# Kernel tuning notes

Measured on AMD Instinct MI355X. Metric: run time of the kernel, lower is better.

## Reference

```python
import jax, jax.numpy as jnp
import numpy as np

B, SQ, SK, D, H = 4, 2048, 2048, 1024, 16
EPS = 1e-6  # flax LayerNorm default


def layer_norm(x, g, b):
    m = x.mean(-1, keepdims=True)
    var = ((x - m) ** 2).mean(-1, keepdims=True)
    return (x - m) * jax.lax.rsqrt(var + EPS) * g + b


def setup_inputs() -> dict:
    key = jax.random.key(0)
    ks = jax.random.split(key, 16)
    s = 1.0 / np.sqrt(D).astype(np.float32)
    inp = {
        'q': jax.random.normal(ks[0], (B, SQ, D), jnp.float32),
        'k': jax.random.normal(ks[1], (B, SK, D), jnp.float32),
        'v': jax.random.normal(ks[2], (B, SK, D), jnp.float32),
        'mask': jax.random.randint(ks[3], (B, SK), 0, 2).astype(bool),
        'Wq': jax.random.normal(ks[4], (D, D), jnp.float32) * s,
        'bq': jnp.zeros((D,), jnp.float32),
        'Wk': jax.random.normal(ks[5], (D, D), jnp.float32) * s,
        'bk': jnp.zeros((D,), jnp.float32),
        'Wv': jax.random.normal(ks[6], (D, D), jnp.float32) * s,
        'bv': jnp.zeros((D,), jnp.float32),
        'Wo': jax.random.normal(ks[7], (D, D), jnp.float32) * s,
        'bo': jnp.zeros((D,), jnp.float32),
        'g1': jnp.ones((D,), jnp.float32),
        'b1': jnp.zeros((D,), jnp.float32),
        'g2': jnp.ones((D,), jnp.float32),
        'b2': jnp.zeros((D,), jnp.float32),
    }
    return inp


def reference(q, k, v, mask, Wq, bq, Wk, bk, Wv, bv, Wo, bo, g1, b1, g2, b2):
    qp = q @ Wq + bq                      # [B, SQ, D]
    kp = k @ Wk + bk                      # [B, SK, D]
    vp = v @ Wv + bv
    qh = qp.reshape(B, SQ, H, D // H)     # head = slice of last dim (matches scatter)
    kh = kp.reshape(B, SK, H, D // H)
    vh = vp.reshape(B, SK, H, D // H)
    # NOTE: original scales by sqrt(dim_out) (full dim), not head dim
    logits = jnp.einsum('bqhd,bkhd->bhqk', qh, kh) / np.sqrt(D).astype(np.float32)
    m = mask[:, None, None, :]            # [B,1,1,SK] broadcast over heads & queries
    A = jax.nn.softmax(jnp.where(m, logits, -jnp.inf), axis=-1)
    A = jnp.where(jnp.isnan(A), 0.0, A)   # fully-masked rows -> 0 (as in original)
    attn = jnp.einsum('bhqk,bkhd->bqhd', A, vh).reshape(B, SQ, D)  # gather heads
    x = layer_norm(qp + attn, g1, b1)
    out = layer_norm(x + jax.nn.relu(x @ Wo + bo), g2, b2)
    return out
```

## Files before the change

### kernel.cpp

```cpp
#include <hip/hip_runtime.h>

#define B_   4
#define SQS  2048
#define SKS  2048
#define DM   1024
#define H_   16
#define MT   8192

typedef __attribute__((ext_vector_type(8))) short bf16x8;
typedef __attribute__((ext_vector_type(4))) float f32x4;

__device__ __forceinline__ float bf2f(unsigned int u) { return __uint_as_float(u << 16); }
__device__ __forceinline__ unsigned short f2bf(float f) {
  unsigned int u = __float_as_uint(f);
  return (unsigned short)((u + 0x7fffu + ((u >> 16) & 1u)) >> 16);
}
__device__ __forceinline__ unsigned int pk_bf16(float a, float b) {
  return __builtin_amdgcn_perm(__float_as_uint(b) + 0x8000u,
                               __float_as_uint(a) + 0x8000u, 0x07060302u);
}
__device__ __forceinline__ unsigned int pk_trunc(float a, float b) {
  return __builtin_amdgcn_perm(__float_as_uint(b), __float_as_uint(a), 0x07060302u);
}
__device__ __forceinline__ float fexp2(float x) {
#if __has_builtin(__builtin_amdgcn_exp2f)
  return __builtin_amdgcn_exp2f(x);
#else
  return __expf(x * 0.69314718056f);
#endif
}
__device__ __forceinline__ void async16(const void* g, void* l) {
  __builtin_amdgcn_global_load_lds((const __attribute__((address_space(1))) unsigned int*)g,
                                   (__attribute__((address_space(3))) unsigned int*)l,
                                   16, 0, 0);
}

#define KSCALE 0.0450842200f
#define BIAS_UNMASKED 0.0028151213f

__global__ __launch_bounds__(256)
void prep_all(const float* __restrict__ q, const float* __restrict__ k,
              const float* __restrict__ v, const int* __restrict__ mask,
              const float* __restrict__ Wq, const float* __restrict__ Wk,
              const float* __restrict__ Wv, const float* __restrict__ Wo,
              unsigned short* __restrict__ qi, unsigned short* __restrict__ ki,
              unsigned short* __restrict__ vi,
              unsigned short* __restrict__ Wqt, unsigned short* __restrict__ Wkt,
              unsigned short* __restrict__ Wvt, unsigned short* __restrict__ Wot,
              float* __restrict__ mskb)
{
  __shared__ float s[32][33];
  const int bx = blockIdx.x, tid = threadIdx.x;
  if (bx < 24576) {
    const int which = bx >> 13, i = bx & 8191;
    const float* src = (which == 0) ? q : (which == 1) ? k : v;
    unsigned short* dst = (which == 0) ? qi : (which == 1) ? ki : vi;
    size_t o = ((size_t)i * 256 + tid) * 4;
    float4 f = *(const float4*)(src + o);
    uint2 u;
    u.x = pk_bf16(f.x, f.y);
    u.y = pk_bf16(f.z, f.w);
    *(uint2*)(dst + o) = u;
  } else if (bx < 28672) {
    const int idx = bx - 24576;
    const int w = idx >> 10, t = idx & 1023;
    const int n0 = (t & 31) * 32, k0 = (t >> 5) * 32;
    const float* W = (w == 0) ? Wq : (w == 1) ? Wk : (w == 2) ? Wv : Wo;
    unsigned short* Wt = (w == 0) ? Wqt : (w == 1) ? Wkt : (w == 2) ? Wvt : Wot;
#pragma unroll
    for (int p = 0; p < 4; p++) {
      int c = p * 256 + tid;
      int r = c >> 5, cc = c & 31;
      s[r][cc] = W[(size_t)(k0 + r) * DM + n0 + cc];
    }
    __syncthreads();
#pragma unroll
    for (int p = 0; p < 4; p++) {
      int c = p * 256 + tid;
      int r = c >> 5, cc = c & 31;
      Wt[(size_t)(n0 + r) * DM + k0 + cc] = f2bf(s[cc][r]);
    }
  } else {
    int i = (bx - 28672) * 256 + tid;
    mskb[i] = mask[i] ? BIAS_UNMASKED : -1e30f;
  }
}

__global__ __launch_bounds__(256)
void qkv_gemm(const unsigned short* __restrict__ A0, const unsigned short* __restrict__ A1,
              const unsigned short* __restrict__ A2,
              const unsigned short* __restrict__ W0, const unsigned short* __restrict__ W1,
              const unsigned short* __restrict__ W2,
              const float* __restrict__ s0, const float* __restrict__ s1,
              const float* __restrict__ s2,
              unsigned short* __restrict__ o0, unsigned short* __restrict__ o1,
              unsigned short* __restrict__ vT)
{
  const int L = blockIdx.x + (blockIdx.y << 3) + (blockIdx.z << 9);
  const int g = L & 7, i5 = L >> 3;
  const int nblk = i5 & 7;
  const int yz = (i5 >> 3) + g * 24;
  const int mblk = yz & 63;
  const int z = yz >> 6;

  const unsigned short* A  = (z == 0) ? A0 : (z == 1) ? A1 : A2;
  const unsigned short* Wt = (z == 0) ? W0 : (z == 1) ? W1 : W2;
  const float* bias        = (z == 0) ? s0 : (z == 1) ? s1 : s2;

  __shared__ short As[128 * 64];
  __shared__ short Bs[128 * 64];
  const int tid = threadIdx.x;
  const int m0 = mblk * 128, n0 = nblk * 128;
  const int wave = tid >> 6, ln = tid & 15, qd = (tid & 63) >> 4;
  const int wm = (wave >> 1) * 64, wn = (wave & 1) * 64;

  int srow[4], sgj[4];
#pragma unroll
  for (int u = 0; u < 4; u++) {
    int c = u * 256 + tid;
    srow[u] = c >> 3;
    sgj[u] = ((c & 7) ^ (srow[u] & 7)) * 8;
  }

  f32x4 acc[4][4];
  const f32x4 vzero = {0.f, 0.f, 0.f, 0.f};
#pragma unroll
  for (int i = 0; i < 4; i++)
#pragma unroll
    for (int j = 0; j < 4; j++) acc[i][j] = vzero;

  for (int k0 = 0; k0 < DM; k0 += 64) {
    __syncthreads();
#pragma unroll
    for (int u = 0; u < 4; u++) {
      int c = u * 256 + tid;
      async16(A  + (size_t)(m0 + srow[u]) * DM + k0 + sgj[u], (char*)As + c * 16);
      async16(Wt + (size_t)(n0 + srow[u]) * DM + k0 + sgj[u], (char*)Bs + c * 16);
    }
    __syncthreads();

#pragma unroll
    for (int kk = 0; kk < 2; kk++) {
      const int ch = ((kk * 4 + qd) ^ (ln & 7)) * 8;
      bf16x8 af[4], bfr[4];
#pragma unroll
      for (int i = 0; i < 4; i++)
        af[i] = *(const bf16x8*)(As + (wm + i * 16 + ln) * 64 + ch);
#pragma unroll
      for (int j = 0; j < 4; j++)
        bfr[j] = *(const bf16x8*)(Bs + (wn + j * 16 + ln) * 64 + ch);
#pragma unroll
      for (int i = 0; i < 4; i++)
#pragma unroll
        for (int j = 0; j < 4; j++)
          acc[i][j] = __builtin_amdgcn_mfma_f32_16x16x32_bf16(af[i], bfr[j], acc[i][j], 0, 0, 0);
    }
  }

  if (z != 2) {
    unsigned short* C = (z == 0) ? o0 : o1;
    const float sc = (z == 1) ? KSCALE : 1.0f;
#pragma unroll
    for (int j = 0; j < 4; j++) {
      int col = n0 + wn + j * 16 + ln;
      float bj = bias[col];
#pragma unroll
      for (int i = 0; i < 4; i++) {
        int row = m0 + wm + i * 16 + qd * 4;
#pragma unroll
        for (int r = 0; r < 4; r++)
          C[(size_t)(row + r) * DM + col] = f2bf((acc[i][j][r] + bj) * sc);
      }
    }
  } else {
#pragma unroll
    for (int j = 0; j < 4; j++) {
      int col = n0 + wn + j * 16 + ln;
      int h = col >> 6, d = col & 63;
      float bj = bias[col];
#pragma unroll
      for (int i = 0; i < 4; i++) {
        int tok0 = m0 + wm + i * 16 + qd * 4;
        int bb = tok0 >> 11;
        int kcol = ((tok0 & 2047) & ~63) + (i & 1) * 32 + qd * 8 + ((i >> 1) & 1) * 4;
        uint2 u;
        u.x = pk_bf16(acc[i][j][0] + bj, acc[i][j][1] + bj);
        u.y = pk_bf16(acc[i][j][2] + bj, acc[i][j][3] + bj);
        *(uint2*)(vT + ((size_t)(bb * H_ + h) * 64 + d) * SKS + kcol) = u;
      }
    }
  }
}

__global__ __launch_bounds__(256)
void gemm_bf16(const unsigned short* __restrict__ A,
               const unsigned short* __restrict__ Wt,
               const float* __restrict__ bias,
               unsigned short* __restrict__ C,
               int relu)
{
  const int L = blockIdx.x + (blockIdx.y << 3);
  const int g = L & 7, i5 = L >> 3;
  const int nblk = i5 & 7;
  const int mblk = (i5 >> 3) + (g << 3);

  __shared__ short As[128 * 64];
  __shared__ short Bs[128 * 64];
  const int tid = threadIdx.x;
  const int m0 = mblk * 128, n0 = nblk * 128;
  const int wave = tid >> 6, ln = tid & 15, qd = (tid & 63) >> 4;
  const int wm = (wave >> 1) * 64, wn = (wave & 1) * 64;

  int srow[4], sgj[4];
#pragma unroll
  for (int u = 0; u < 4; u++) {
    int c = u * 256 + tid;
    srow[u] = c >> 3;
    sgj[u] = ((c & 7) ^ (srow[u] & 7)) * 8;
  }

  f32x4 acc[4][4];
  const f32x4 vzero = {0.f, 0.f, 0.f, 0.f};
#pragma unroll
  for (int i = 0; i < 4; i++)
#pragma unroll
    for (int j = 0; j < 4; j++) acc[i][j] = vzero;

  for (int k0 = 0; k0 < DM; k0 += 64) {
    __syncthreads();
#pragma unroll
    for (int u = 0; u < 4; u++) {
      int c = u * 256 + tid;
      async16(A  + (size_t)(m0 + srow[u]) * DM + k0 + sgj[u], (char*)As + c * 16);
      async16(Wt + (size_t)(n0 + srow[u]) * DM + k0 + sgj[u], (char*)Bs + c * 16);
    }
    __syncthreads();

#pragma unroll
    for (int kk = 0; kk < 2; kk++) {
      const int ch = ((kk * 4 + qd) ^ (ln & 7)) * 8;
      bf16x8 af[4], bfr[4];
#pragma unroll
      for (int i = 0; i < 4; i++)
        af[i] = *(const bf16x8*)(As + (wm + i * 16 + ln) * 64 + ch);
#pragma unroll
      for (int j = 0; j < 4; j++)
        bfr[j] = *(const bf16x8*)(Bs + (wn + j * 16 + ln) * 64 + ch);
#pragma unroll
      for (int i = 0; i < 4; i++)
#pragma unroll
        for (int j = 0; j < 4; j++)
          acc[i][j] = __builtin_amdgcn_mfma_f32_16x16x32_bf16(af[i], bfr[j], acc[i][j], 0, 0, 0);
    }
  }

#pragma unroll
  for (int j = 0; j < 4; j++) {
    int col = n0 + wn + j * 16 + ln;
    float bj = bias[col];
#pragma unroll
    for (int i = 0; i < 4; i++) {
      int row = m0 + wm + i * 16 + qd * 4;
#pragma unroll
      for (int r = 0; r < 4; r++) {
        float v = acc[i][j][r] + bj;
        if (relu) v = fmaxf(v, 0.f);
        C[(size_t)(row + r) * DM + col] = f2bf(v);
      }
    }
  }
}

__global__ __launch_bounds__(256, 2)
void attn_fwd(const unsigned short* __restrict__ qp,
              const unsigned short* __restrict__ kp,
              const unsigned short* __restrict__ vT,
              const float* __restrict__ maskb,
              unsigned short* __restrict__ attn)
{
  __shared__ short Ks[128 * 64];
  __shared__ short Vs[64 * 128];
  __shared__ float bias_s[128];

  const int tid = threadIdx.x;
  const int L = blockIdx.x + (blockIdx.y << 3) + (blockIdx.z << 7);
  const int g = L & 7, i5 = L >> 3;
  const int qblk = i5 & 7;
  const int bh = (i5 >> 3) + (g << 3);
  const int h = bh & 15, b = bh >> 4;
  const int q0 = qblk * 256;
  const int wave = tid >> 6, ln = tid & 15, qd = (tid & 63) >> 4;

  int kRow[4], kOff[4], vRow[4], vOff[4];
#pragma unroll
  for (int u = 0; u < 4; u++) {
    int c = u * 256 + tid;
    kRow[u] = c >> 3;
    kOff[u] = ((c & 7) ^ (kRow[u] & 7)) * 8;
    vRow[u] = c >> 4;
    int j = c & 15;
    vOff[u] = ((j & 8) | ((j ^ vRow[u]) & 7)) * 8;
  }

  const unsigned short* kbase = kp + (size_t)(b * SKS) * DM + (h << 6);
  const unsigned short* vbase = vT + (size_t)((b * H_ + h) * 64) * SKS;

  bf16x8 qf[4][2];
#pragma unroll
  for (int gq = 0; gq < 4; gq++) {
    const unsigned short* qrow =
        qp + (size_t)(b * SQS + q0 + wave * 64 + gq * 16 + ln) * DM + (h << 6);
    qf[gq][0] = *(const bf16x8*)(qrow + qd * 8);
    qf[gq][1] = *(const bf16x8*)(qrow + 32 + qd * 8);
  }

  union { bf16x8 v; unsigned int u[4]; } onesf;
  onesf.u[0] = onesf.u[1] = onesf.u[2] = onesf.u[3] = 0x3F803F80u;

  const f32x4 vzero = {0.f, 0.f, 0.f, 0.f};
  f32x4 oA[4][4], lacc[4];
#pragma unroll
  for (int gq = 0; gq < 4; gq++) {
    lacc[gq] = vzero;
#pragma unroll
    for (int t = 0; t < 4; t++) oA[gq][t] = vzero;
  }

  for (int kt = 0; kt < SKS / 128; kt++) {
    const int k0 = kt * 128;
    __syncthreads();
    if (tid < 128) bias_s[tid] = maskb[b * SKS + k0 + tid];
#pragma unroll
    for (int u = 0; u < 4; u++) {
      int c = u * 256 + tid;
      async16(kbase + (size_t)(k0 + kRow[u]) * DM + kOff[u], (char*)Ks + c * 16);
      async16(vbase + (size_t)vRow[u] * SKS + k0 + vOff[u], (char*)Vs + c * 16);
    }
    __syncthreads();

#pragma unroll
    for (int h2 = 0; h2 < 2; h2++) {
      bf16x8 kf[4][2];
      f32x4 btv[4];
#pragma unroll
      for (int t = 0; t < 4; t++) {
        const short* krow = Ks + (h2 * 64 + t * 16 + ln) * 64;
        kf[t][0] = *(const bf16x8*)(krow + ((0 + qd) ^ (ln & 7)) * 8);
        kf[t][1] = *(const bf16x8*)(krow + ((4 + qd) ^ (ln & 7)) * 8);
        btv[t] = *(const f32x4*)(bias_s + h2 * 64 + t * 16 + qd * 4);
      }

      bf16x8 pf[4][2];
#pragma unroll
      for (int gq = 0; gq < 4; gq++) {
        f32x4 sS[4];
#pragma unroll
        for (int t = 0; t < 4; t++) {
          f32x4 a = __builtin_amdgcn_mfma_f32_16x16x32_bf16(kf[t][0], qf[gq][0], btv[t], 0, 0, 0);
          sS[t]   = __builtin_amdgcn_mfma_f32_16x16x32_bf16(kf[t][1], qf[gq][1], a,      0, 0, 0);
        }
        float p[4][4];
#pragma unroll
        for (int t = 0; t < 4; t++) {
          p[t][0] = fexp2(sS[t][0]);
          p[t][1] = fexp2(sS[t][1]);
          p[t][2] = fexp2(sS[t][2]);
          p[t][3] = fexp2(sS[t][3]);
        }
        union { bf16x8 v; unsigned int u[4]; } P0, P1;
        P0.u[0] = pk_trunc(p[0][0], p[0][1]);
        P0.u[1] = pk_trunc(p[0][2], p[0][3]);
        P0.u[2] = pk_trunc(p[2][0], p[2][1]);
        P0.u[3] = pk_trunc(p[2][2], p[2][3]);
        P1.u[0] = pk_trunc(p[1][0], p[1][1]);
        P1.u[1] = pk_trunc(p[1][2], p[1][3]);
        P1.u[2] = pk_trunc(p[3][0], p[3][1]);
        P1.u[3] = pk_trunc(p[3][2], p[3][3]);
        pf[gq][0] = P0.v;
        pf[gq][1] = P1.v;
        lacc[gq] = __builtin_amdgcn_mfma_f32_16x16x32_bf16(pf[gq][0], onesf.v, lacc[gq], 0, 0, 0);
        lacc[gq] = __builtin_amdgcn_mfma_f32_16x16x32_bf16(pf[gq][1], onesf.v, lacc[gq], 0, 0, 0);
      }

#pragma unroll
      for (int t2 = 0; t2 < 4; t2++) {
        const short* vrow = Vs + (t2 * 16 + ln) * 128;
        bf16x8 vf0 = *(const bf16x8*)(vrow + (h2 * 8 + ((0 + qd) ^ (ln & 7))) * 8);
        bf16x8 vf1 = *(const bf16x8*)(vrow + (h2 * 8 + ((4 + qd) ^ (ln & 7))) * 8);
#pragma unroll
        for (int gq = 0; gq < 4; gq++) {
          oA[gq][t2] = __builtin_amdgcn_mfma_f32_16x16x32_bf16(pf[gq][0], vf0, oA[gq][t2], 0, 0, 0);
          oA[gq][t2] = __builtin_amdgcn_mfma_f32_16x16x32_bf16(pf[gq][1], vf1, oA[gq][t2], 0, 0, 0);
        }
      }
    }
  }

#pragma unroll
  for (int gq = 0; gq < 4; gq++) {
    float linv[4];
#pragma unroll
    for (int r = 0; r < 4; r++)
      linv[r] = (lacc[gq][r] > 0.f) ? 1.0f / lacc[gq][r] : 0.f;
#pragma unroll
    for (int t2 = 0; t2 < 4; t2++)
#pragma unroll
      for (int r = 0; r < 4; r++) {
        size_t idx = (size_t)(b * SQS + q0 + wave * 64 + gq * 16 + qd * 4 + r) * DM
                   + (h << 6) + t2 * 16 + ln;
        attn[idx] = f2bf(oA[gq][t2][r] * linv[r]);
      }
  }
}

__global__ __launch_bounds__(256)
void ln_fuse(const unsigned short* __restrict__ Xa, const unsigned short* __restrict__ Xb,
             const float* __restrict__ gamma, const float* __restrict__ beta,
             unsigned short* __restrict__ outb, float* __restrict__ outf, int mode)
{
  const int row = blockIdx.x, tid = threadIdx.x;
  const size_t base = (size_t)row * DM + tid * 4;
  uint2 ua = *(const uint2*)(Xa + base);
  uint2 ub = *(const uint2*)(Xb + base);
  float v0 = bf2f(ua.x & 0xffffu) + bf2f(ub.x & 0xffffu);
  float v1 = bf2f(ua.x >> 16)     + bf2f(ub.x >> 16);
  float v2 = bf2f(ua.y & 0xffffu) + bf2f(ub.y & 0xffffu);
  float v3 = bf2f(ua.y >> 16)     + bf2f(ub.y >> 16);
  float s  = (v0 + v1) + (v2 + v3);
  float s2 = (v0 * v0 + v1 * v1) + (v2 * v2 + v3 * v3);
#pragma unroll
  for (int off = 1; off < 64; off <<= 1) {
    s  += __shfl_xor(s, off);
    s2 += __shfl_xor(s2, off);
  }
  __shared__ float red[8];
  if ((tid & 63) == 0) { red[tid >> 6] = s; red[4 + (tid >> 6)] = s2; }
  __syncthreads();
  float S  = (red[0] + red[1]) + (red[2] + red[3]);
  float S2 = (red[4] + red[5]) + (red[6] + red[7]);
  float mean = S * (1.0f / 1024.0f);
  float var  = S2 * (1.0f / 1024.0f) - mean * mean;
  float rstd = rsqrtf(var + 1e-6f);
  int c = tid * 4;
  float o0 = (v0 - mean) * rstd * gamma[c + 0] + beta[c + 0];
  float o1 = (v1 - mean) * rstd * gamma[c + 1] + beta[c + 1];
  float o2 = (v2 - mean) * rstd * gamma[c + 2] + beta[c + 2];
  float o3 = (v3 - mean) * rstd * gamma[c + 3] + beta[c + 3];
  if (mode == 0) {
    uint2 o;
    o.x = (unsigned)f2bf(o0) | ((unsigned)f2bf(o1) << 16);
    o.y = (unsigned)f2bf(o2) | ((unsigned)f2bf(o3) << 16);
    *(uint2*)(outb + base) = o;
  } else {
    float4 o = {o0, o1, o2, o3};
    *(float4*)(outf + base) = o;
  }
}

extern "C" void kernel_launch(void* const* d_in, const int* in_sizes, int n_in,
                              void* d_out, int out_size, void* d_ws, size_t ws_size,
                              hipStream_t stream)
{
  (void)in_sizes; (void)n_in; (void)out_size; (void)ws_size;
  const float* q    = (const float*)d_in[0];
  const float* k    = (const float*)d_in[1];
  const float* v    = (const float*)d_in[2];
  const int*   mask = (const int*)  d_in[3];
  const float* Wq   = (const float*)d_in[4];
  const float* bq   = (const float*)d_in[5];
  const float* Wk   = (const float*)d_in[6];
  const float* bk   = (const float*)d_in[7];
  const float* Wv   = (const float*)d_in[8];
  const float* bv   = (const float*)d_in[9];
  const float* Wo   = (const float*)d_in[10];
  const float* bo   = (const float*)d_in[11];
  const float* g1   = (const float*)d_in[12];
  const float* b1   = (const float*)d_in[13];
  const float* g2   = (const float*)d_in[14];
  const float* b2   = (const float*)d_in[15];

  char* ws = (char*)d_ws;
  const size_t SZ16 = (size_t)16 << 20;
  unsigned short* qi   = (unsigned short*)(ws + 0 * SZ16);
  unsigned short* ki   = (unsigned short*)(ws + 1 * SZ16);
  unsigned short* vi   = (unsigned short*)(ws + 2 * SZ16);
  unsigned short* qpb  = (unsigned short*)(ws + 3 * SZ16);
  unsigned short* kpb  = (unsigned short*)(ws + 4 * SZ16);
  unsigned short* vTb  = (unsigned short*)(ws + 6 * SZ16);
  unsigned short* Wqt  = (unsigned short*)(ws + 7 * SZ16 + ((size_t)0 << 20));
  unsigned short* Wkt  = (unsigned short*)(ws + 7 * SZ16 + ((size_t)2 << 20));
  unsigned short* Wvt  = (unsigned short*)(ws + 7 * SZ16 + ((size_t)4 << 20));
  unsigned short* Wot  = (unsigned short*)(ws + 7 * SZ16 + ((size_t)6 << 20));
  float*          mskb = (float*)         (ws + 7 * SZ16 + ((size_t)8 << 20));
  unsigned short* attnb = qi;
  unsigned short* xb    = ki;
  unsigned short* hb    = vi;

  prep_all     <<<28704,            256, 0, stream>>>(q, k, v, mask, Wq, Wk, Wv, Wo,
                                                      qi, ki, vi, Wqt, Wkt, Wvt, Wot, mskb);

  qkv_gemm     <<<dim3(8, 64, 3),   256, 0, stream>>>(qi, ki, vi, Wqt, Wkt, Wvt,
                                                      bq, bk, bv, qpb, kpb, vTb);

  attn_fwd     <<<dim3(8, 16, 4),   256, 0, stream>>>(qpb, kpb, vTb, mskb, attnb);

  ln_fuse      <<<8192,             256, 0, stream>>>(qpb, attnb, g1, b1, xb, nullptr, 0);
  gemm_bf16    <<<dim3(8, 64),      256, 0, stream>>>(xb, Wot, bo, hb, 1);
  ln_fuse      <<<8192,             256, 0, stream>>>(xb, hb, g2, b2, nullptr, (float*)d_out, 1);
}
```

Before: 347.4 us.

## Split attention over two key halves and merge partials in layernorm

The attention kernel now splits the key sequence into two halves, launching twice as many blocks. Each block writes an unnormalized bf16 partial output and its row sums to workspace. The first layernorm kernel becomes a merge kernel that adds both partials, divides by the combined sum and applies layernorm. This is meant to raise parallelism and occupancy in attention (launch bounds raised to 4 blocks per CU), at the cost of extra partial-output traffic. Since no running max is used, the partials combine exactly, but rounding the unnormalized partials to bf16 may lose some precision.

After: 759.1 us. 119% more time.

```diff
diff --git a/kernel.cpp b/kernel.cpp
--- a/kernel.cpp
+++ b/kernel.cpp
@@ -271,24 +271,28 @@
   }
 }
 
-__global__ __launch_bounds__(256, 2)
+__global__ __launch_bounds__(256, 4)
 void attn_fwd(const unsigned short* __restrict__ qp,
               const unsigned short* __restrict__ kp,
               const unsigned short* __restrict__ vT,
               const float* __restrict__ maskb,
-              unsigned short* __restrict__ attn)
+              unsigned short* __restrict__ O0,
+              unsigned short* __restrict__ O1,
+              float* __restrict__ lws)
 {
   __shared__ short Ks[128 * 64];
   __shared__ short Vs[64 * 128];
   __shared__ float bias_s[128];
 
   const int tid = threadIdx.x;
-  const int L = blockIdx.x + (blockIdx.y << 3) + (blockIdx.z << 7);
+  const int L = blockIdx.x + (blockIdx.y << 4) + (blockIdx.z << 8);
   const int g = L & 7, i5 = L >> 3;
-  const int qblk = i5 & 7;
-  const int bh = (i5 >> 3) + (g << 3);
+  const int half = i5 & 1;
+  const int qblk = (i5 >> 1) & 7;
+  const int bh = (i5 >> 4) + (g << 3);
   const int h = bh & 15, b = bh >> 4;
   const int q0 = qblk * 256;
+  const int koff0 = half * (SKS / 2);
   const int wave = tid >> 6, ln = tid & 15, qd = (tid & 63) >> 4;
 
   int kRow[4], kOff[4], vRow[4], vOff[4];
@@ -326,8 +330,8 @@
     for (int t = 0; t < 4; t++) oA[gq][t] = vzero;
   }
 
-  for (int kt = 0; kt < SKS / 128; kt++) {
-    const int k0 = kt * 128;
+  for (int kt = 0; kt < SKS / 2 / 128; kt++) {
+    const int k0 = koff0 + kt * 128;
     __syncthreads();
     if (tid < 128) bias_s[tid] = maskb[b * SKS + k0 + tid];
 #pragma unroll
@@ -396,36 +400,49 @@
     }
   }
 
+  unsigned short* obuf = half ? O1 : O0;
+  float* lbuf = lws + (size_t)half * (B_ * H_ * SQS);
 #pragma unroll
   for (int gq = 0; gq < 4; gq++) {
-    float linv[4];
-#pragma unroll
-    for (int r = 0; r < 4; r++)
-      linv[r] = (lacc[gq][r] > 0.f) ? 1.0f / lacc[gq][r] : 0.f;
+    int qloc = q0 + wave * 64 + gq * 16 + qd * 4;
+    if (ln == 0) {
+#pragma unroll
+      for (int r = 0; r < 4; r++)
+        lbuf[(size_t)(b * H_ + h) * SQS + qloc + r] = lacc[gq][r];
+    }
 #pragma unroll
     for (int t2 = 0; t2 < 4; t2++)
 #pragma unroll
       for (int r = 0; r < 4; r++) {
-        size_t idx = (size_t)(b * SQS + q0 + wave * 64 + gq * 16 + qd * 4 + r) * DM
-                   + (h << 6) + t2 * 16 + ln;
-        attn[idx] = f2bf(oA[gq][t2][r] * linv[r]);
+        size_t idx = (size_t)(b * SQS + qloc + r) * DM + (h << 6) + t2 * 16 + ln;
+        obuf[idx] = f2bf(oA[gq][t2][r]);
       }
   }
 }
 
 __global__ __launch_bounds__(256)
-void ln_fuse(const unsigned short* __restrict__ Xa, const unsigned short* __restrict__ Xb,
-             const float* __restrict__ gamma, const float* __restrict__ beta,
-             unsigned short* __restrict__ outb, float* __restrict__ outf, int mode)
+void ln_merge(const unsigned short* __restrict__ Xa, const unsigned short* __restrict__ O0,
+              const unsigned short* __restrict__ O1, const float* __restrict__ lws,
+              const float* __restrict__ gamma, const float* __restrict__ beta,
+              unsigned short* __restrict__ outb)
 {
   const int row = blockIdx.x, tid = threadIdx.x;
+  const int b = row >> 11, q = row & 2047;
+  const int h = tid >> 4;
+  const size_t lidx = (size_t)(b * H_ + h) * SQS + q;
+  float la = lws[lidx], lb2 = lws[lidx + (size_t)(B_ * H_ * SQS)];
+  float lsum = la + lb2;
+  float linv = (lsum > 0.f) ? 1.0f / lsum : 0.f;
+
   const size_t base = (size_t)row * DM + tid * 4;
   uint2 ua = *(const uint2*)(Xa + base);
-  uint2 ub = *(const uint2*)(Xb + base);
-  float v0 = bf2f(ua.x & 0xffffu) + bf2f(ub.x & 0xffffu);
-  float v1 = bf2f(ua.x >> 16)     + bf2f(ub.x >> 16);
-  float v2 = bf2f(ua.y & 0xffffu) + bf2f(ub.y & 0xffffu);
-  float v3 = bf2f(ua.y >> 16)     + bf2f(ub.y >> 16);
+  uint2 u0 = *(const uint2*)(O0 + base);
+  uint2 u1 = *(const uint2*)(O1 + base);
+  float v0 = bf2f(ua.x & 0xffffu) + (bf2f(u0.x & 0xffffu) + bf2f(u1.x & 0xffffu)) * linv;
+  float v1 = bf2f(ua.x >> 16)     + (bf2f(u0.x >> 16)     + bf2f(u1.x >> 16))     * linv;
+  float v2 = bf2f(ua.y & 0xffffu) + (bf2f(u0.y & 0xffffu) + bf2f(u1.y & 0xffffu)) * linv;
+  float v3 = bf2f(ua.y >> 16)     + (bf2f(u0.y >> 16)     + bf2f(u1.y >> 16))     * linv;
+
   float s  = (v0 + v1) + (v2 + v3);
   float s2 = (v0 * v0 + v1 * v1) + (v2 * v2 + v3 * v3);
 #pragma unroll
@@ -446,15 +463,47 @@
   float o1 = (v1 - mean) * rstd * gamma[c + 1] + beta[c + 1];
   float o2 = (v2 - mean) * rstd * gamma[c + 2] + beta[c + 2];
   float o3 = (v3 - mean) * rstd * gamma[c + 3] + beta[c + 3];
-  if (mode == 0) {
-    uint2 o;
-    o.x = (unsigned)f2bf(o0) | ((unsigned)f2bf(o1) << 16);
-    o.y = (unsigned)f2bf(o2) | ((unsigned)f2bf(o3) << 16);
-    *(uint2*)(outb + base) = o;
-  } else {
-    float4 o = {o0, o1, o2, o3};
-    *(float4*)(outf + base) = o;
-  }
+  uint2 o;
+  o.x = pk_bf16(o0, o1);
+  o.y = pk_bf16(o2, o3);
+  *(uint2*)(outb + base) = o;
+}
+
+__global__ __launch_bounds__(256)
+void ln_fuse(const unsigned short* __restrict__ Xa, const unsigned short* __restrict__ Xb,
+             const float* __restrict__ gamma, const float* __restrict__ beta,
+             float* __restrict__ outf)
+{
+  const int row = blockIdx.x, tid = threadIdx.x;
+  const size_t base = (size_t)row * DM + tid * 4;
+  uint2 ua = *(const uint2*)(Xa + base);
+  uint2 ub = *(const uint2*)(Xb + base);
+  float v0 = bf2f(ua.x & 0xffffu) + bf2f(ub.x & 0xffffu);
+  float v1 = bf2f(ua.x >> 16)     + bf2f(ub.x >> 16);
+  float v2 = bf2f(ua.y & 0xffffu) + bf2f(ub.y & 0xffffu);
+  float v3 = bf2f(ua.y >> 16)     + bf2f(ub.y >> 16);
+  float s  = (v0 + v1) + (v2 + v3);
+  float s2 = (v0 * v0 + v1 * v1) + (v2 * v2 + v3 * v3);
+#pragma unroll
+  for (int off = 1; off < 64; off <<= 1) {
+    s  += __shfl_xor(s, off);
+    s2 += __shfl_xor(s2, off);
+  }
+  __shared__ float red[8];
+  if ((tid & 63) == 0) { red[tid >> 6] = s; red[4 + (tid >> 6)] = s2; }
+  __syncthreads();
+  float S  = (red[0] + red[1]) + (red[2] + red[3]);
+  float S2 = (red[4] + red[5]) + (red[6] + red[7]);
+  float mean = S * (1.0f / 1024.0f);
+  float var  = S2 * (1.0f / 1024.0f) - mean * mean;
+  float rstd = rsqrtf(var + 1e-6f);
+  int c = tid * 4;
+  float o0 = (v0 - mean) * rstd * gamma[c + 0] + beta[c + 0];
+  float o1 = (v1 - mean) * rstd * gamma[c + 1] + beta[c + 1];
+  float o2 = (v2 - mean) * rstd * gamma[c + 2] + beta[c + 2];
+  float o3 = (v3 - mean) * rstd * gamma[c + 3] + beta[c + 3];
+  float4 o = {o0, o1, o2, o3};
+  *(float4*)(outf + base) = o;
 }
 
 extern "C" void kernel_launch(void* const* d_in, const int* in_sizes, int n_in,
@@ -492,9 +541,11 @@
   unsigned short* Wvt  = (unsigned short*)(ws + 7 * SZ16 + ((size_t)4 << 20));
   unsigned short* Wot  = (unsigned short*)(ws + 7 * SZ16 + ((size_t)6 << 20));
   float*          mskb = (float*)         (ws + 7 * SZ16 + ((size_t)8 << 20));
-  unsigned short* attnb = qi;
-  unsigned short* xb    = ki;
-  unsigned short* hb    = vi;
+  float*          lws  = (float*)         (ws + 7 * SZ16 + ((size_t)9 << 20));
+  unsigned short* O0b  = qi;
+  unsigned short* O1b  = vi;
+  unsigned short* xb   = ki;
+  unsigned short* hb   = vTb;
 
   prep_all     <<<28704,            256, 0, stream>>>(q, k, v, mask, Wq, Wk, Wv, Wo,
                                                       qi, ki, vi, Wqt, Wkt, Wvt, Wot, mskb);
@@ -502,9 +553,9 @@
   qkv_gemm     <<<dim3(8, 64, 3),   256, 0, stream>>>(qi, ki, vi, Wqt, Wkt, Wvt,
                                                       bq, bk, bv, qpb, kpb, vTb);
 
-  attn_fwd     <<<dim3(8, 16, 4),   256, 0, stream>>>(qpb, kpb, vTb, mskb, attnb);
-
-  ln_fuse      <<<8192,             256, 0, stream>>>(qpb, attnb, g1, b1, xb, nullptr, 0);
+  attn_fwd     <<<dim3(16, 16, 4),  256, 0, stream>>>(qpb, kpb, vTb, mskb, O0b, O1b, lws);
+
+  ln_merge     <<<8192,             256, 0, stream>>>(qpb, O0b, O1b, lws, g1, b1, xb);
   gemm_bf16    <<<dim3(8, 64),      256, 0, stream>>>(xb, Wot, bo, hb, 1);
-  ln_fuse      <<<8192,             256, 0, stream>>>(xb, hb, g2, b2, nullptr, (float*)d_out, 1);
-}
+  ln_fuse      <<<8192,             256, 0, stream>>>(xb, hb, g2, b2, (float*)d_out);
+}
```

## Load K/V fragments directly from global memory in attention, dropping LDS staging

Applied to the files above, without the earlier changes.

The attention kernel no longer stages K, V and mask-bias tiles through shared memory with async copies and two barriers per tile. Each wave now loads its K, V and bias MFMA fragments straight from global memory, 64 keys per step, and the launch-bounds occupancy hint is removed. This removes LDS traffic and block-wide syncs, but each of the four waves loads the same K/V data redundantly and relies on cache hits, with no prefetch overlap. The LayerNorm bf16 packing also switches to the cheaper perm-based pack helper.

Measured after the change: 403.5 us. +16.1%, slower.

```diff
diff --git a/kernel.cpp b/kernel.cpp
--- a/kernel.cpp
+++ b/kernel.cpp
@@ -271,17 +271,13 @@
   }
 }
 
-__global__ __launch_bounds__(256, 2)
+__global__ __launch_bounds__(256)
 void attn_fwd(const unsigned short* __restrict__ qp,
               const unsigned short* __restrict__ kp,
               const unsigned short* __restrict__ vT,
               const float* __restrict__ maskb,
               unsigned short* __restrict__ attn)
 {
-  __shared__ short Ks[128 * 64];
-  __shared__ short Vs[64 * 128];
-  __shared__ float bias_s[128];
-
   const int tid = threadIdx.x;
   const int L = blockIdx.x + (blockIdx.y << 3) + (blockIdx.z << 7);
   const int g = L & 7, i5 = L >> 3;
@@ -291,19 +287,9 @@
   const int q0 = qblk * 256;
   const int wave = tid >> 6, ln = tid & 15, qd = (tid & 63) >> 4;
 
-  int kRow[4], kOff[4], vRow[4], vOff[4];
-#pragma unroll
-  for (int u = 0; u < 4; u++) {
-    int c = u * 256 + tid;
-    kRow[u] = c >> 3;
-    kOff[u] = ((c & 7) ^ (kRow[u] & 7)) * 8;
-    vRow[u] = c >> 4;
-    int j = c & 15;
-    vOff[u] = ((j & 8) | ((j ^ vRow[u]) & 7)) * 8;
-  }
-
   const unsigned short* kbase = kp + (size_t)(b * SKS) * DM + (h << 6);
   const unsigned short* vbase = vT + (size_t)((b * H_ + h) * 64) * SKS;
+  const float* bbase = maskb + b * SKS;
 
   bf16x8 qf[4][2];
 #pragma unroll
@@ -326,72 +312,63 @@
     for (int t = 0; t < 4; t++) oA[gq][t] = vzero;
   }
 
-  for (int kt = 0; kt < SKS / 128; kt++) {
-    const int k0 = kt * 128;
-    __syncthreads();
-    if (tid < 128) bias_s[tid] = maskb[b * SKS + k0 + tid];
-#pragma unroll
-    for (int u = 0; u < 4; u++) {
-      int c = u * 256 + tid;
-      async16(kbase + (size_t)(k0 + kRow[u]) * DM + kOff[u], (char*)Ks + c * 16);
-      async16(vbase + (size_t)vRow[u] * SKS + k0 + vOff[u], (char*)Vs + c * 16);
-    }
-    __syncthreads();
-
-#pragma unroll
-    for (int h2 = 0; h2 < 2; h2++) {
-      bf16x8 kf[4][2];
-      f32x4 btv[4];
+  for (int kt = 0; kt < SKS / 64; kt++) {
+    const int kb = kt * 64;
+
+    bf16x8 kf[4][2], vf[4][2];
+    f32x4 btv[4];
+#pragma unroll
+    for (int t = 0; t < 4; t++) {
+      const unsigned short* krow = kbase + (size_t)(kb + t * 16 + ln) * DM;
+      kf[t][0] = *(const bf16x8*)(krow + qd * 8);
+      kf[t][1] = *(const bf16x8*)(krow + 32 + qd * 8);
+      btv[t] = *(const f32x4*)(bbase + kb + t * 16 + qd * 4);
+    }
+#pragma unroll
+    for (int t2 = 0; t2 < 4; t2++) {
+      const unsigned short* vrow = vbase + (size_t)(t2 * 16 + ln) * SKS + kb;
+      vf[t2][0] = *(const bf16x8*)(vrow + qd * 8);
+      vf[t2][1] = *(const bf16x8*)(vrow + 32 + qd * 8);
+    }
+
+    bf16x8 pf[4][2];
+#pragma unroll
+    for (int gq = 0; gq < 4; gq++) {
+      f32x4 sS[4];
 #pragma unroll
       for (int t = 0; t < 4; t++) {
-        const short* krow = Ks + (h2 * 64 + t * 16 + ln) * 64;
-        kf[t][0] = *(const bf16x8*)(krow + ((0 + qd) ^ (ln & 7)) * 8);
-        kf[t][1] = *(const bf16x8*)(krow + ((4 + qd) ^ (ln & 7)) * 8);
-        btv[t] = *(const f32x4*)(bias_s + h2 * 64 + t * 16 + qd * 4);
-      }
-
-      bf16x8 pf[4][2];
+        f32x4 a = __builtin_amdgcn_mfma_f32_16x16x32_bf16(kf[t][0], qf[gq][0], btv[t], 0, 0, 0);
+        sS[t]   = __builtin_amdgcn_mfma_f32_16x16x32_bf16(kf[t][1], qf[gq][1], a,      0, 0, 0);
+      }
+      float p[4][4];
+#pragma unroll
+      for (int t = 0; t < 4; t++) {
+        p[t][0] = fexp2(sS[t][0]);
+        p[t][1] = fexp2(sS[t][1]);
+        p[t][2] = fexp2(sS[t][2]);
+        p[t][3] = fexp2(sS[t][3]);
+      }
+      union { bf16x8 v; unsigned int u[4]; } P0, P1;
+      P0.u[0] = pk_trunc(p[0][0], p[0][1]);
+      P0.u[1] = pk_trunc(p[0][2], p[0][3]);
+      P0.u[2] = pk_trunc(p[2][0], p[2][1]);
+      P0.u[3] = pk_trunc(p[2][2], p[2][3]);
+      P1.u[0] = pk_trunc(p[1][0], p[1][1]);
+      P1.u[1] = pk_trunc(p[1][2], p[1][3]);
+      P1.u[2] = pk_trunc(p[3][0], p[3][1]);
+      P1.u[3] = pk_trunc(p[3][2], p[3][3]);
+      pf[gq][0] = P0.v;
+      pf[gq][1] = P1.v;
+      lacc[gq] = __builtin_amdgcn_mfma_f32_16x16x32_bf16(pf[gq][0], onesf.v, lacc[gq], 0, 0, 0);
+      lacc[gq] = __builtin_amdgcn_mfma_f32_16x16x32_bf16(pf[gq][1], onesf.v, lacc[gq], 0, 0, 0);
+    }
+
+#pragma unroll
+    for (int t2 = 0; t2 < 4; t2++) {
 #pragma unroll
       for (int gq = 0; gq < 4; gq++) {
-        f32x4 sS[4];
-#pragma unroll
-        for (int t = 0; t < 4; t++) {
-          f32x4 a = __builtin_amdgcn_mfma_f32_16x16x32_bf16(kf[t][0], qf[gq][0], btv[t], 0, 0, 0);
-          sS[t]   = __builtin_amdgcn_mfma_f32_16x16x32_bf16(kf[t][1], qf[gq][1], a,      0, 0, 0);
-        }
-        float p[4][4];
-#pragma unroll
-        for (int t = 0; t < 4; t++) {
-          p[t][0] = fexp2(sS[t][0]);
-          p[t][1] = fexp2(sS[t][1]);
-          p[t][2] = fexp2(sS[t][2]);
-          p[t][3] = fexp2(sS[t][3]);
-        }
-        union { bf16x8 v; unsigned int u[4]; } P0, P1;
-        P0.u[0] = pk_trunc(p[0][0], p[0][1]);
-        P0.u[1] = pk_trunc(p[0][2], p[0][3]);
-        P0.u[2] = pk_trunc(p[2][0], p[2][1]);
-        P0.u[3] = pk_trunc(p[2][2], p[2][3]);
-        P1.u[0] = pk_trunc(p[1][0], p[1][1]);
-        P1.u[1] = pk_trunc(p[1][2], p[1][3]);
-        P1.u[2] = pk_trunc(p[3][0], p[3][1]);
-        P1.u[3] = pk_trunc(p[3][2], p[3][3]);
-        pf[gq][0] = P0.v;
-        pf[gq][1] = P1.v;
-        lacc[gq] = __builtin_amdgcn_mfma_f32_16x16x32_bf16(pf[gq][0], onesf.v, lacc[gq], 0, 0, 0);
-        lacc[gq] = __builtin_amdgcn_mfma_f32_16x16x32_bf16(pf[gq][1], onesf.v, lacc[gq], 0, 0, 0);
-      }
-
-#pragma unroll
-      for (int t2 = 0; t2 < 4; t2++) {
-        const short* vrow = Vs + (t2 * 16 + ln) * 128;
-        bf16x8 vf0 = *(const bf16x8*)(vrow + (h2 * 8 + ((0 + qd) ^ (ln & 7))) * 8);
-        bf16x8 vf1 = *(const bf16x8*)(vrow + (h2 * 8 + ((4 + qd) ^ (ln & 7))) * 8);
-#pragma unroll
-        for (int gq = 0; gq < 4; gq++) {
-          oA[gq][t2] = __builtin_amdgcn_mfma_f32_16x16x32_bf16(pf[gq][0], vf0, oA[gq][t2], 0, 0, 0);
-          oA[gq][t2] = __builtin_amdgcn_mfma_f32_16x16x32_bf16(pf[gq][1], vf1, oA[gq][t2], 0, 0, 0);
-        }
+        oA[gq][t2] = __builtin_amdgcn_mfma_f32_16x16x32_bf16(pf[gq][0], vf[t2][0], oA[gq][t2], 0, 0, 0);
+        oA[gq][t2] = __builtin_amdgcn_mfma_f32_16x16x32_bf16(pf[gq][1], vf[t2][1], oA[gq][t2], 0, 0, 0);
       }
     }
   }
@@ -448,8 +425,8 @@
   float o3 = (v3 - mean) * rstd * gamma[c + 3] + beta[c + 3];
   if (mode == 0) {
     uint2 o;
-    o.x = (unsigned)f2bf(o0) | ((unsigned)f2bf(o1) << 16);
-    o.y = (unsigned)f2bf(o2) | ((unsigned)f2bf(o3) << 16);
+    o.x = pk_bf16(o0, o1);
+    o.y = pk_bf16(o2, o3);
     *(uint2*)(outb + base) = o;
   } else {
     float4 o = {o0, o1, o2, o3};
```
